# Kernel optimization log

Hardware: AMD Instinct MI355X
Metric: run time of the kernel (lower is better)

Reference implementation:

```python
import jax, jax.numpy as jnp
import numpy as np

EPS = 1e-5


def _ligru_layer(x, W, U, gamma, beta):
    """One bidirectional LiGRU layer. x: (B,T,F) -> (B,T,2H)."""
    B = x.shape[0]
    H = U.shape[1]
    # bidirectional: stack forward copy and time-flipped copy along batch
    x2 = jnp.concatenate([x, x[:, ::-1]], axis=0)  # (2B, T, F)
    w = jnp.einsum('btf,gf->btg', x2, W)           # (2B, T, 2H)
    # training-mode BatchNorm1d over flattened (2B*T, 2H), biased variance
    flat = w.reshape(-1, w.shape[-1])
    mean = flat.mean(axis=0)
    var = flat.var(axis=0)
    w = (w - mean) * jax.lax.rsqrt(var + EPS) * gamma + beta

    def step(h, wt):
        gates = wt + h @ U.T            # (2B, 2H)
        at, zt = gates[:, :H], gates[:, H:]
        z = jax.nn.sigmoid(zt)
        h = z * h + (1.0 - z) * jax.nn.relu(at)
        return h, h

    h0 = jnp.zeros((w.shape[0], H), dtype=w.dtype)
    _, hs = jax.lax.scan(step, h0, jnp.swapaxes(w, 0, 1))  # (T, 2B, H)
    hs = jnp.swapaxes(hs, 0, 1)                            # (2B, T, H)
    h_f, h_b = hs[:B], hs[B:, ::-1]                        # un-flip backward dir
    return jnp.concatenate([h_f, h_b], axis=2)             # (B, T, 2H)


def setup_inputs() -> dict:
    key = jax.random.key(0)
    ks = jax.random.split(key, 9)
    B, T, F, H = 16, 500, 512, 1024
    return {
        'x': jax.random.normal(ks[0], (B, T, F), jnp.float32),
        'w0': jax.random.normal(ks[1], (2 * H, F), jnp.float32) * (1.0 / np.sqrt(F)),
        'u0': jax.random.normal(ks[2], (2 * H, H), jnp.float32) * (1.0 / np.sqrt(H)),
        'g0': jax.random.uniform(ks[3], (2 * H,), jnp.float32, 0.5, 1.5),
        'b0': jax.random.normal(ks[4], (2 * H,), jnp.float32) * 0.1,
        'w1': jax.random.normal(ks[5], (2 * H, 2 * H), jnp.float32) * (1.0 / np.sqrt(2 * H)),
        'u1': jax.random.normal(ks[6], (2 * H, H), jnp.float32) * (1.0 / np.sqrt(H)),
        'g1': jax.random.uniform(ks[7], (2 * H,), jnp.float32, 0.5, 1.5),
        'b1': jax.random.normal(ks[8], (2 * H,), jnp.float32) * 0.1,
    }


def reference(x, w0, u0, g0, b0, w1, u1, g1, b1):
    h = _ligru_layer(x, w0, u0, g0, b0)   # (B, T, 2H)
    h = _ligru_layer(h, w1, u1, g1, b1)   # (B, T, 2H)
    return h
```

## Files before the change

kernel.cpp:

```cpp
#include <hip/hip_runtime.h>
#include <stdint.h>

#define KT 500
#define KH 1024
#define KG 2048
#define FPAD 16

typedef short bf16x8 __attribute__((ext_vector_type(8)));
typedef float f32x4 __attribute__((ext_vector_type(4)));

__device__ __forceinline__ unsigned short f2bf(float f){
  union { float f; unsigned int i; } u; u.f = f;
  unsigned int x = u.i;
  return (unsigned short)((x + 0x7fffu + ((x >> 16) & 1u)) >> 16);
}
__device__ __forceinline__ float bf2f(unsigned short h){
  union { unsigned int i; float f; } u; u.i = ((unsigned int)h) << 16;
  return u.f;
}

template<int OFF>
__device__ __forceinline__ void load_b128_dev_off(uint4& dst, const void* p){
  asm volatile("global_load_dwordx4 %0, %1, off offset:%c2 sc1"
               : "=v"(dst) : "v"(p), "i"(OFF) : "memory");
}
__device__ __forceinline__ void store_b32_dev(void* p, unsigned int v){
  asm volatile("global_store_dword %0, %1, off sc1"
               :: "v"(p), "v"(v) : "memory");
}
__device__ __forceinline__ void wait_vm0(){
  asm volatile("s_waitcnt vmcnt(0)" ::: "memory");
}
__device__ __forceinline__ void wait_vm8(){
  asm volatile("s_waitcnt vmcnt(8)" ::: "memory");
}

__global__ __launch_bounds__(256) void castk(const float* __restrict__ s,
                                             unsigned short* __restrict__ d, int n4){
  int i = blockIdx.x*256 + threadIdx.x;
  if (i >= n4) return;
  float4 v = ((const float4*)s)[i];
  unsigned int lo = (unsigned int)f2bf(v.x) | ((unsigned int)f2bf(v.y) << 16);
  unsigned int hi = (unsigned int)f2bf(v.z) | ((unsigned int)f2bf(v.w) << 16);
  ((uint2*)d)[i] = make_uint2(lo, hi);
}

template<int MODE, int KDIM>
__global__ __launch_bounds__(256) void gemm_bn(
    const unsigned short* __restrict__ A,
    const unsigned short* __restrict__ Bw,
    unsigned short* __restrict__ Wout)
{
  __shared__ __attribute__((aligned(16))) unsigned short As[128*72];
  __shared__ __attribute__((aligned(16))) unsigned short Bs[128*72];
  const int tid = threadIdx.x;
  const int lane = tid & 63, wid = tid >> 6;
  const int ntile = blockIdx.x, mtile = blockIdx.y;
  const int arow_loc = tid >> 3;
  const int k8 = tid & 7;

  long abaseLo[4], abaseHi[4], bbase[4];
  #pragma unroll
  for (int i = 0; i < 4; i++){
    int r = mtile*128 + i*32 + arow_loc;
    int s = r / KT;
    int t = r - s*KT;
    if (MODE == 0){
      abaseLo[i] = (s < 16) ? (long)((s*KT + t)*512)
                            : (long)(((s-16)*KT + (KT-1-t))*512);
      abaseHi[i] = 0;
    } else {
      int sp = s & 15;
      int rev = (s >= 16);
      abaseLo[i] = (long)((sp*KT + (rev ? KT-1-t : t)) * KH);
      abaseHi[i] = (long)(((16+sp)*KT + (rev ? t : KT-1-t)) * KH);
    }
    bbase[i] = (long)(ntile*128 + i*32 + arow_loc) * KDIM;
  }

  f32x4 acc[4][4];
  #pragma unroll
  for (int a=0;a<4;a++)
    #pragma unroll
    for (int b=0;b<4;b++)
      acc[a][b] = (f32x4){0.f,0.f,0.f,0.f};

  const int mhalf = wid & 1, nhalf = wid >> 1;
  const int lrow = lane & 15, quad = lane >> 4;

  for (int k0 = 0; k0 < KDIM; k0 += 64){
    const int kel = k0 + k8*8;
    #pragma unroll
    for (int i = 0; i < 4; i++){
      long aoff;
      if (MODE == 0) aoff = abaseLo[i] + kel;
      else           aoff = (kel < KH) ? (abaseLo[i] + kel) : (abaseHi[i] + (kel - KH));
      uint4 va = *(const uint4*)(A + aoff);
      uint4 vb = *(const uint4*)(Bw + bbase[i] + kel);
      *(uint4*)&As[(i*32 + arow_loc)*72 + k8*8] = va;
      *(uint4*)&Bs[(i*32 + arow_loc)*72 + k8*8] = vb;
    }
    __syncthreads();
    #pragma unroll
    for (int kk = 0; kk < 64; kk += 32){
      bf16x8 af[4], bfr[4];
      #pragma unroll
      for (int mt=0; mt<4; mt++)
        af[mt] = *(const bf16x8*)&As[(mhalf*64 + mt*16 + lrow)*72 + kk + quad*8];
      #pragma unroll
      for (int nt=0; nt<4; nt++)
        bfr[nt] = *(const bf16x8*)&Bs[(nhalf*64 + nt*16 + lrow)*72 + kk + quad*8];
      #pragma unroll
      for (int mt=0; mt<4; mt++)
        #pragma unroll
        for (int nt=0; nt<4; nt++)
          acc[mt][nt] = __builtin_amdgcn_mfma_f32_16x16x32_bf16(af[mt], bfr[nt], acc[mt][nt], 0, 0, 0);
    }
    __syncthreads();
  }

  #pragma unroll
  for (int mt=0; mt<4; mt++)
    #pragma unroll
    for (int nt=0; nt<4; nt++)
      #pragma unroll
      for (int r=0; r<4; r++){
        int grow = mtile*128 + mhalf*64 + mt*16 + quad*4 + r;
        int gcol = ntile*128 + nhalf*64 + nt*16 + lrow;
        Wout[(long)grow*KG + gcol] = f2bf(acc[mt][nt][r]);
      }
}

__global__ __launch_bounds__(256) void bn_partial(const unsigned short* __restrict__ W,
                                                  float* __restrict__ part){
  const int blk = blockIdx.x, tid = threadIdx.x;
  const int c0 = tid*8;
  float s[8], qq[8];
  #pragma unroll
  for (int j=0;j<8;j++){ s[j]=0.f; qq[j]=0.f; }
  const unsigned short* base = W + (long)blk*128*KG + c0;
  for (int r=0;r<128;r++){
    uint4 v = *(const uint4*)(base + (long)r*KG);
    unsigned int w[4] = {v.x, v.y, v.z, v.w};
    #pragma unroll
    for (int p=0;p<4;p++){
      union { unsigned int i; float f; } lo, hi;
      lo.i = w[p] << 16;
      hi.i = w[p] & 0xffff0000u;
      s[2*p]   += lo.f; qq[2*p]   += lo.f*lo.f;
      s[2*p+1] += hi.f; qq[2*p+1] += hi.f*hi.f;
    }
  }
  float* pd = part + (long)blk*4096;
  #pragma unroll
  for (int j=0;j<8;j++){ pd[c0+j] = s[j]; pd[KG + c0 + j] = qq[j]; }
}

__global__ __launch_bounds__(256) void bn_final(const float* __restrict__ part,
                                                const float* __restrict__ gamma,
                                                const float* __restrict__ beta,
                                                float* __restrict__ scsh){
  int g = blockIdx.x*256 + threadIdx.x;
  float s=0.f, qq=0.f;
  for (int b=0;b<125;b++){ s += part[(long)b*4096 + g]; qq += part[(long)b*4096 + KG + g]; }
  float mean = s * (1.f/16000.f);
  float var  = qq * (1.f/16000.f) - mean*mean;
  float sc = gamma[g] * rsqrtf(var + 1e-5f);
  scsh[g]      = sc;
  scsh[KG + g] = beta[g] - mean*sc;
}

template<int LAYER>
__global__ __launch_bounds__(256, 1) void recur(
    const unsigned short* __restrict__ Ub,
    const unsigned short* __restrict__ Wn,
    const float* __restrict__ scsh,
    unsigned short* __restrict__ hbuf,
    int* __restrict__ flags,
    unsigned short* __restrict__ hsOut,
    float* __restrict__ out)
{
  __shared__ float gA0[32*20];
  __shared__ float gZ0[32*20];
  __shared__ float gA1[32*20];
  __shared__ float gZ1[32*20];

  const int tid = threadIdx.x;
  const int q = blockIdx.x;
  const int ga = q*16;
  const int lane = tid & 63, wid = tid >> 6;
  const int lrow = lane & 15, quad = lane >> 4;
  const int m = wid & 1, kh = wid >> 1;
  const int es = tid >> 3, ep = tid & 7;

  bf16x8 ufA[16], ufZ[16];
  {
    const unsigned short* ua = Ub + (long)(ga + lrow)*KH + kh*512 + quad*8;
    const unsigned short* uz = ua + (long)KH*KH;
    #pragma unroll
    for (int c=0;c<16;c++){
      ufA[c] = *(const bf16x8*)(ua + c*32);
      asm volatile("" : "+a"(ufA[c]));
      ufZ[c] = *(const bf16x8*)(uz + c*32);
      asm volatile("" : "+a"(ufZ[c]));
    }
  }

  float2 scav = *(const float2*)&scsh[ga + 2*ep];
  float2 shav = *(const float2*)&scsh[KG + ga + 2*ep];
  float2 sczv = *(const float2*)&scsh[KH + ga + 2*ep];
  float2 shzv = *(const float2*)&scsh[KG + KH + ga + 2*ep];
  float2 hprev = make_float2(0.f, 0.f);

  const long aoff = (long)(m*16 + lrow)*KH + kh*512 + quad*8;
  const unsigned short* hb0 = hbuf + aoff;
  const unsigned short* hb1 = hbuf + 32768 + aoff;

  for (int t = 0; t < KT; t++){
    const unsigned short* wr = Wn + (long)(es*KT + t)*KG + ga + 2*ep;
    unsigned int wa01 = *(const unsigned int*)(wr);
    unsigned int wz01 = *(const unsigned int*)(wr + KH);
    asm volatile("" ::: "memory");

    if (t > 0){
      if (lane < 32){
        const int* fp = &flags[(kh*32 + lane) << 4];
        while (__hip_atomic_load(fp, __ATOMIC_RELAXED,
                                 __HIP_MEMORY_SCOPE_AGENT) < t){}
      }
    } else {
      wait_vm0();
    }

    const unsigned short* hb = (t & 1) ? hb1 : hb0;
    uint4 af[16];
    #define LDAF(i) load_b128_dev_off<(i)*64>(af[i], hb)
    LDAF(0);  LDAF(1);  LDAF(2);  LDAF(3);
    LDAF(4);  LDAF(5);  LDAF(6);  LDAF(7);
    LDAF(8);  LDAF(9);  LDAF(10); LDAF(11);
    LDAF(12); LDAF(13); LDAF(14); LDAF(15);
    #undef LDAF

    f32x4 aA0 = (f32x4){0,0,0,0}, aA1 = aA0, aZ0 = aA0, aZ1 = aA0;

    wait_vm8();
    __builtin_amdgcn_sched_barrier(0);
    #pragma unroll
    for (int c=0;c<8;c+=2){
      bf16x8 x0 = *(bf16x8*)&af[c];
      bf16x8 x1 = *(bf16x8*)&af[c+1];
      aA0 = __builtin_amdgcn_mfma_f32_16x16x32_bf16(x0, ufA[c],   aA0, 0,0,0);
      aZ0 = __builtin_amdgcn_mfma_f32_16x16x32_bf16(x0, ufZ[c],   aZ0, 0,0,0);
      aA1 = __builtin_amdgcn_mfma_f32_16x16x32_bf16(x1, ufA[c+1], aA1, 0,0,0);
      aZ1 = __builtin_amdgcn_mfma_f32_16x16x32_bf16(x1, ufZ[c+1], aZ1, 0,0,0);
    }
    wait_vm0();
    __builtin_amdgcn_sched_barrier(0);
    #pragma unroll
    for (int c=8;c<16;c+=2){
      bf16x8 x0 = *(bf16x8*)&af[c];
      bf16x8 x1 = *(bf16x8*)&af[c+1];
      aA0 = __builtin_amdgcn_mfma_f32_16x16x32_bf16(x0, ufA[c],   aA0, 0,0,0);
      aZ0 = __builtin_amdgcn_mfma_f32_16x16x32_bf16(x0, ufZ[c],   aZ0, 0,0,0);
      aA1 = __builtin_amdgcn_mfma_f32_16x16x32_bf16(x1, ufA[c+1], aA1, 0,0,0);
      aZ1 = __builtin_amdgcn_mfma_f32_16x16x32_bf16(x1, ufZ[c+1], aZ1, 0,0,0);
    }
    f32x4 accA = aA0 + aA1;
    f32x4 accZ = aZ0 + aZ1;

    {
      float* gAd = kh ? gA1 : gA0;
      float* gZd = kh ? gZ1 : gZ0;
      #pragma unroll
      for (int r=0;r<4;r++){
        gAd[(m*16 + quad*4 + r)*20 + lrow] = accA[r];
        gZd[(m*16 + quad*4 + r)*20 + lrow] = accZ[r];
      }
    }
    __syncthreads();

    float2 ga0 = *(const float2*)&gA0[es*20 + 2*ep];
    float2 ga1 = *(const float2*)&gA1[es*20 + 2*ep];
    float2 gz0 = *(const float2*)&gZ0[es*20 + 2*ep];
    float2 gz1 = *(const float2*)&gZ1[es*20 + 2*ep];
    float aa0 = ga0.x + ga1.x + bf2f((unsigned short)(wa01 & 0xffff)) * scav.x + shav.x;
    float aa1 = ga0.y + ga1.y + bf2f((unsigned short)(wa01 >> 16))    * scav.y + shav.y;
    float zz0 = gz0.x + gz1.x + bf2f((unsigned short)(wz01 & 0xffff)) * sczv.x + shzv.x;
    float zz1 = gz0.y + gz1.y + bf2f((unsigned short)(wz01 >> 16))    * sczv.y + shzv.y;
    float z0 = 1.f/(1.f + __expf(-zz0));
    float z1 = 1.f/(1.f + __expf(-zz1));
    float hn0 = z0*hprev.x + (1.f - z0)*fmaxf(aa0, 0.f);
    float hn1 = z1*hprev.y + (1.f - z1)*fmaxf(aa1, 0.f);
    hprev = make_float2(hn0, hn1);

    unsigned int hpack = (unsigned int)f2bf(hn0) | ((unsigned int)f2bf(hn1) << 16);

    if (LAYER == 0){
      *(unsigned int*)&hsOut[(long)(es*KT + t)*KH + ga + 2*ep] = hpack;
    } else {
      if (es < 16)
        *(float2*)&out[(long)(es*KT + t)*KG + ga + 2*ep] = make_float2(hn0, hn1);
      else
        *(float2*)&out[(long)((es-16)*KT + (KT-1-t))*KG + KH + ga + 2*ep] = make_float2(hn0, hn1);
    }

    store_b32_dev(hbuf + ((t+1)&1)*32768 + es*KH + ga + 2*ep, hpack);
    wait_vm0();
    __syncthreads();
    if (tid == 0)
      __hip_atomic_store(&flags[q << 4], t + 1, __ATOMIC_RELAXED,
                         __HIP_MEMORY_SCOPE_AGENT);
  }
}

extern "C" void kernel_launch(void* const* d_in, const int* in_sizes, int n_in,
                              void* d_out, int out_size, void* d_ws, size_t ws_size,
                              hipStream_t stream)
{
  const float* x  = (const float*)d_in[0];
  const float* w0 = (const float*)d_in[1];
  const float* u0 = (const float*)d_in[2];
  const float* g0 = (const float*)d_in[3];
  const float* b0 = (const float*)d_in[4];
  const float* w1 = (const float*)d_in[5];
  const float* u1 = (const float*)d_in[6];
  const float* g1 = (const float*)d_in[7];
  const float* b1 = (const float*)d_in[8];
  float* out = (float*)d_out;

  char* p = (char*)d_ws;
  auto alloc = [&](size_t n){ char* r = p; p += (n + 255) & ~(size_t)255; return r; };
  unsigned short* xb   = (unsigned short*)alloc((size_t)16*KT*512*2);
  unsigned short* w0b  = (unsigned short*)alloc((size_t)KG*512*2);
  unsigned short* u0b  = (unsigned short*)alloc((size_t)KG*KH*2);
  unsigned short* w1b  = (unsigned short*)alloc((size_t)KG*KG*2);
  unsigned short* u1b  = (unsigned short*)alloc((size_t)KG*KH*2);
  unsigned short* wbuf = (unsigned short*)alloc((size_t)32*KT*KG*2);
  unsigned short* hs0  = (unsigned short*)alloc((size_t)32*KT*KH*2);
  float* part          = (float*)alloc((size_t)125*4096*4);
  float* scsh          = (float*)alloc((size_t)2*KG*4);
  unsigned short* hbuf = (unsigned short*)alloc((size_t)2*2*32*KH*2);
  int* flags           = (int*)alloc((size_t)2*64*FPAD*4);

  auto cast = [&](const float* s, unsigned short* d, int n){
    int n4 = n >> 2;
    castk<<<(n4+255)/256, 256, 0, stream>>>(s, d, n4);
  };
  cast(x,  xb,  16*KT*512);
  cast(w0, w0b, KG*512);
  cast(u0, u0b, KG*KH);
  cast(w1, w1b, KG*KG);
  cast(u1, u1b, KG*KH);
  hipMemsetAsync(hbuf,  0, (size_t)2*2*32*KH*2, stream);
  hipMemsetAsync(flags, 0, (size_t)2*64*FPAD*4, stream);

  gemm_bn<0,512><<<dim3(16,125), 256, 0, stream>>>(xb, w0b, wbuf);
  bn_partial<<<125,256,0,stream>>>(wbuf, part);
  bn_final<<<8,256,0,stream>>>(part, g0, b0, scsh);
  recur<0><<<64,256,0,stream>>>(u0b, wbuf, scsh, hbuf, flags, hs0, (float*)nullptr);

  gemm_bn<1,2048><<<dim3(16,125), 256, 0, stream>>>(hs0, w1b, wbuf);
  bn_partial<<<125,256,0,stream>>>(wbuf, part);
  bn_final<<<8,256,0,stream>>>(part, g1, b1, scsh);
  recur<1><<<64,256,0,stream>>>(u1b, wbuf, scsh, hbuf + 2*32*KH, flags + 64*FPAD,
                                (unsigned short*)nullptr, out);
}
```

Measured before the change: 4.263 ms.

## Use per-wave flags for finer-grained cross-block recurrence synchronization

```diff
diff --git a/kernel.cpp b/kernel.cpp
--- a/kernel.cpp
+++ b/kernel.cpp
@@ -180,10 +180,10 @@
     unsigned short* __restrict__ hsOut,
     float* __restrict__ out)
 {
-  __shared__ float gA0[32*20];
-  __shared__ float gZ0[32*20];
-  __shared__ float gA1[32*20];
-  __shared__ float gZ1[32*20];
+  __shared__ float gA0[2][32*20];
+  __shared__ float gZ0[2][32*20];
+  __shared__ float gA1[2][32*20];
+  __shared__ float gZ1[2][32*20];
 
   const int tid = threadIdx.x;
   const int q = blockIdx.x;
@@ -216,6 +216,10 @@
   const unsigned short* hb0 = hbuf + aoff;
   const unsigned short* hb1 = hbuf + 32768 + aoff;
 
+  const int pp = kh*32 + (lane >> 1);
+  const int pw = 2*m + (lane & 1);
+  const int* fpoll = &flags[((pp*4 + pw)) << 4];
+
   for (int t = 0; t < KT; t++){
     const unsigned short* wr = Wn + (long)(es*KT + t)*KG + ga + 2*ep;
     unsigned int wa01 = *(const unsigned int*)(wr);
@@ -223,11 +227,8 @@
     asm volatile("" ::: "memory");
 
     if (t > 0){
-      if (lane < 32){
-        const int* fp = &flags[(kh*32 + lane) << 4];
-        while (__hip_atomic_load(fp, __ATOMIC_RELAXED,
-                                 __HIP_MEMORY_SCOPE_AGENT) < t){}
-      }
+      while (__hip_atomic_load(fpoll, __ATOMIC_RELAXED,
+                               __HIP_MEMORY_SCOPE_AGENT) < t){}
     } else {
       wait_vm0();
     }
@@ -268,9 +269,10 @@
     f32x4 accA = aA0 + aA1;
     f32x4 accZ = aZ0 + aZ1;
 
+    const int par = t & 1;
     {
-      float* gAd = kh ? gA1 : gA0;
-      float* gZd = kh ? gZ1 : gZ0;
+      float* gAd = kh ? gA1[par] : gA0[par];
+      float* gZd = kh ? gZ1[par] : gZ0[par];
       #pragma unroll
       for (int r=0;r<4;r++){
         gAd[(m*16 + quad*4 + r)*20 + lrow] = accA[r];
@@ -279,14 +281,14 @@
     }
     __syncthreads();
 
-    float2 ga0 = *(const float2*)&gA0[es*20 + 2*ep];
-    float2 ga1 = *(const float2*)&gA1[es*20 + 2*ep];
-    float2 gz0 = *(const float2*)&gZ0[es*20 + 2*ep];
-    float2 gz1 = *(const float2*)&gZ1[es*20 + 2*ep];
-    float aa0 = ga0.x + ga1.x + bf2f((unsigned short)(wa01 & 0xffff)) * scav.x + shav.x;
-    float aa1 = ga0.y + ga1.y + bf2f((unsigned short)(wa01 >> 16))    * scav.y + shav.y;
-    float zz0 = gz0.x + gz1.x + bf2f((unsigned short)(wz01 & 0xffff)) * sczv.x + shzv.x;
-    float zz1 = gz0.y + gz1.y + bf2f((unsigned short)(wz01 >> 16))    * sczv.y + shzv.y;
+    float2 va0 = *(const float2*)&gA0[par][es*20 + 2*ep];
+    float2 va1 = *(const float2*)&gA1[par][es*20 + 2*ep];
+    float2 vz0 = *(const float2*)&gZ0[par][es*20 + 2*ep];
+    float2 vz1 = *(const float2*)&gZ1[par][es*20 + 2*ep];
+    float aa0 = va0.x + va1.x + bf2f((unsigned short)(wa01 & 0xffff)) * scav.x + shav.x;
+    float aa1 = va0.y + va1.y + bf2f((unsigned short)(wa01 >> 16))    * scav.y + shav.y;
+    float zz0 = vz0.x + vz1.x + bf2f((unsigned short)(wz01 & 0xffff)) * sczv.x + shzv.x;
+    float zz1 = vz0.y + vz1.y + bf2f((unsigned short)(wz01 >> 16))    * sczv.y + shzv.y;
     float z0 = 1.f/(1.f + __expf(-zz0));
     float z1 = 1.f/(1.f + __expf(-zz1));
     float hn0 = z0*hprev.x + (1.f - z0)*fmaxf(aa0, 0.f);
@@ -295,6 +297,7 @@
 
     unsigned int hpack = (unsigned int)f2bf(hn0) | ((unsigned int)f2bf(hn1) << 16);
 
+    store_b32_dev(hbuf + ((t+1)&1)*32768 + es*KH + ga + 2*ep, hpack);
     if (LAYER == 0){
       *(unsigned int*)&hsOut[(long)(es*KT + t)*KH + ga + 2*ep] = hpack;
     } else {
@@ -304,11 +307,9 @@
         *(float2*)&out[(long)((es-16)*KT + (KT-1-t))*KG + KH + ga + 2*ep] = make_float2(hn0, hn1);
     }
 
-    store_b32_dev(hbuf + ((t+1)&1)*32768 + es*KH + ga + 2*ep, hpack);
     wait_vm0();
-    __syncthreads();
-    if (tid == 0)
-      __hip_atomic_store(&flags[q << 4], t + 1, __ATOMIC_RELAXED,
+    if (lane == 0)
+      __hip_atomic_store(&flags[(q*4 + wid) << 4], t + 1, __ATOMIC_RELAXED,
                          __HIP_MEMORY_SCOPE_AGENT);
   }
 }
@@ -340,7 +341,7 @@
   float* part          = (float*)alloc((size_t)125*4096*4);
   float* scsh          = (float*)alloc((size_t)2*KG*4);
   unsigned short* hbuf = (unsigned short*)alloc((size_t)2*2*32*KH*2);
-  int* flags           = (int*)alloc((size_t)2*64*FPAD*4);
+  int* flags           = (int*)alloc((size_t)2*64*4*FPAD*4);
 
   auto cast = [&](const float* s, unsigned short* d, int n){
     int n4 = n >> 2;
@@ -352,7 +353,7 @@
   cast(w1, w1b, KG*KG);
   cast(u1, u1b, KG*KH);
   hipMemsetAsync(hbuf,  0, (size_t)2*2*32*KH*2, stream);
-  hipMemsetAsync(flags, 0, (size_t)2*64*FPAD*4, stream);
+  hipMemsetAsync(flags, 0, (size_t)2*64*4*FPAD*4, stream);
 
   gemm_bn<0,512><<<dim3(16,125), 256, 0, stream>>>(xb, w0b, wbuf);
   bn_partial<<<125,256,0,stream>>>(wbuf, part);
@@ -362,6 +363,6 @@
   gemm_bn<1,2048><<<dim3(16,125), 256, 0, stream>>>(hs0, w1b, wbuf);
   bn_partial<<<125,256,0,stream>>>(wbuf, part);
   bn_final<<<8,256,0,stream>>>(part, g1, b1, scsh);
-  recur<1><<<64,256,0,stream>>>(u1b, wbuf, scsh, hbuf + 2*32*KH, flags + 64*FPAD,
+  recur<1><<<64,256,0,stream>>>(u1b, wbuf, scsh, hbuf + 2*32*KH, flags + 64*4*FPAD,
                                 (unsigned short*)nullptr, out);
 }
```

Result: no change. 4.304 ms (+1.0%).
